# Kernel optimization log

Hardware: AMD Instinct MI355X
Metric: run time of the kernel (lower is better)

Reference implementation:

```python
import jax, jax.numpy as jnp
from jax import lax
import numpy as np

B, CIN, HC, K, REC = 64, 64, 64, 3, 5
MG = 240 // REC  # 48
EPS = 1e-8


def conv2d(x, w, b, pad):
    y = lax.conv_general_dilated(x, w, (1, 1), [(pad, pad), (pad, pad)],
                                 dimension_numbers=('NCHW', 'OIHW', 'NCHW'))
    return y + b[None, :, None, None]


def conv_transpose2d(x, w, b, stride, pad):
    # PyTorch ConvTranspose2d: w is (Cin, Cout, kH, kW)
    k = w.shape[2]
    w_t = jnp.transpose(w[:, :, ::-1, ::-1], (1, 0, 2, 3))  # -> OIHW, flipped
    y = lax.conv_general_dilated(x, w_t, (1, 1),
                                 [(k - 1 - pad, k - 1 - pad)] * 2,
                                 lhs_dilation=(stride, stride),
                                 dimension_numbers=('NCHW', 'OIHW', 'NCHW'))
    return y + b[None, :, None, None]


def leaky(x):
    return jnp.where(x >= 0, x, 0.2 * x)


def setup_inputs() -> dict:
    key = jax.random.key(0)
    ks = jax.random.split(key, 12)
    s = 0.05
    return {
        'x': jax.random.normal(ks[0], (B, CIN, 64, 64), jnp.float32),
        'h': jax.random.normal(ks[1], (B, HC, 64, 64), jnp.float32),
        'c': jax.random.normal(ks[2], (B, HC, 64, 64), jnp.float32),
        'recalled_memory_feature': jax.random.normal(ks[3], (B, REC, MG, 32, 32), jnp.float32),
        'conv_w': jax.random.normal(ks[4], (5 * HC, CIN + HC, K, K), jnp.float32) * s,
        'conv_b': jax.random.normal(ks[5], (5 * HC,), jnp.float32) * s,
        'convc_w': jax.random.normal(ks[6], (MG, HC, 1, 1), jnp.float32) * s,
        'convc_b': jax.random.normal(ks[7], (MG,), jnp.float32) * s,
        'convssm_w': jax.random.normal(ks[8], (MG, MG, 4, 4), jnp.float32) * s,
        'convssm_b': jax.random.normal(ks[9], (MG,), jnp.float32) * s,
        'convfuse_w': jax.random.normal(ks[10], (HC, MG + HC, 1, 1), jnp.float32) * s,
        'convfuse_b': jax.random.normal(ks[11], (HC,), jnp.float32) * s,
    }


def reference(x, h, c, recalled_memory_feature, conv_w, conv_b, convc_w, convc_b,
              convssm_w, convssm_b, convfuse_w, convfuse_b):
    rm = recalled_memory_feature.reshape(B, REC, MG, 32, 32)
    rm_avg = rm.mean(axis=(3, 4))                      # (B, REC, MG)
    q = leaky(conv2d(c, convc_w, convc_b, 0))          # (B, MG, 64, 64)
    q_avg = q.mean(axis=(2, 3))                        # (B, MG)
    # cosine similarity along channel dim, vectorized over (B, REC)
    qn = jnp.maximum(jnp.linalg.norm(q_avg, axis=1, keepdims=True), EPS)   # (B,1)
    mn = jnp.maximum(jnp.linalg.norm(rm_avg, axis=2), EPS)                  # (B,REC)
    cos = jnp.einsum('bm,brm->br', q_avg, rm_avg) / (qn * mn)               # (B,REC)
    attn = jax.nn.softmax(cos, axis=1)                                      # (B,REC)
    mt = jnp.einsum('br,brmhw->bmhw', attn, rm)        # (B, MG, 32, 32)
    mt = leaky(conv_transpose2d(mt, convssm_w, convssm_b, 2, 1))  # (B, MG, 64, 64)

    gates = conv2d(jnp.concatenate((x, h), axis=1), conv_w, conv_b, K // 2)
    i, f, g, o, lam = jnp.split(gates, 5, axis=1)
    i = jax.nn.sigmoid(i)
    f = jax.nn.sigmoid(f)
    o = jax.nn.sigmoid(o)
    g = jnp.tanh(g)
    lam = jax.nn.sigmoid(lam)
    c_new = f * c + i * g
    h_new = o * jnp.tanh(conv2d(jnp.concatenate((c_new, mt), axis=1), convfuse_w, convfuse_b, 0))
    h_out = lam * h_new + (1.0 - lam) * h
    return (h_out, c_new)
```

## Files before the change

### kernel.cpp

```cpp
#include <hip/hip_runtime.h>
#include <hip/hip_bf16.h>
#include <cstdint>

#define HW 4096
#define MGc 48
#define RECc 5

typedef __attribute__((ext_vector_type(8))) short bf16x8;
typedef __attribute__((ext_vector_type(4))) float f32x4;

__device__ __forceinline__ float sigf(float x) { return 1.f / (1.f + expf(-x)); }
__device__ __forceinline__ float leakyf(float x) { return x >= 0.f ? x : 0.2f * x; }
__device__ __forceinline__ unsigned short f2bfu(float f) {
  __hip_bfloat16 b = __float2bfloat16(f);
  return *reinterpret_cast<unsigned short*>(&b);
}
__device__ __forceinline__ float bfu2f(unsigned short u) {
  unsigned v = ((unsigned)u) << 16;
  return __uint_as_float(v);
}
__device__ __forceinline__ void gload_lds16(const void* g, void* l) {
  __builtin_amdgcn_global_load_lds(
      (const __attribute__((address_space(1))) unsigned int*)g,
      (__attribute__((address_space(3))) unsigned int*)l, 16, 0, 0);
}

__global__ __launch_bounds__(256) void k_prep(const float* __restrict__ cw,
    __hip_bfloat16* __restrict__ Wp, __hip_bfloat16* __restrict__ Pp) {
  if (blockIdx.x < 1440) {
    int idx = blockIdx.x * 256 + threadIdx.x;
    int t = idx / (320 * 128);
    int rem = idx % (320 * 128);
    int ocp = rem / 128, ci = rem % 128;
    int nt = ocp / 80, r2 = ocp % 80, gate = r2 / 16, ml = r2 % 16;
    int oc = gate * 64 + nt * 16 + ml;
    Wp[idx] = __float2bfloat16(cw[((size_t)oc * 128 + ci) * 9 + t]);
  } else {
    int idx = (blockIdx.x - 1440) * 256 + threadIdx.x;
    int b = idx / 4160, i = idx % 4160;
    bf16x8* base = reinterpret_cast<bf16x8*>(Pp);
    size_t u;
    if (i < 2112) {
      int r = (i < 1056) ? 0 : 65;
      int j = (i < 1056) ? i : i - 1056;
      u = ((size_t)b * 66 + r) * 1056 + j;
    } else {
      int i2 = i - 2112;
      int row = 1 + (i2 >> 5), k = i2 & 31;
      int px = (k < 16) ? 0 : 65, ci8 = k & 15;
      u = (((size_t)b * 66 + row) * 66 + px) * 16 + ci8;
    }
    base[u] = (bf16x8)0;
  }
}

__global__ __launch_bounds__(256) void k_rm_sum(const float* __restrict__ rm,
                                                float* __restrict__ rm_sum) {
  int row = blockIdx.x;
  const float4* p = reinterpret_cast<const float4*>(rm + (size_t)row * 1024);
  float4 v = p[threadIdx.x];
  float s = v.x + v.y + v.z + v.w;
  #pragma unroll
  for (int off = 32; off; off >>= 1) s += __shfl_down(s, off);
  __shared__ float sred[4];
  if ((threadIdx.x & 63) == 0) sred[threadIdx.x >> 6] = s;
  __syncthreads();
  if (threadIdx.x == 0) rm_sum[row] = sred[0] + sred[1] + sred[2] + sred[3];
}

__global__ __launch_bounds__(256) void k_q_part(const float* __restrict__ c,
    const float* __restrict__ ccw, const float* __restrict__ ccb,
    float* __restrict__ q_part) {
  __shared__ float wl[MGc * 64];
  __shared__ float bl[MGc];
  __shared__ float red[4][MGc];
  int b = blockIdx.y, seg = blockIdx.x;
  for (int i = threadIdx.x; i < MGc * 64; i += 256) wl[i] = ccw[i];
  if (threadIdx.x < MGc) bl[threadIdx.x] = ccb[threadIdx.x];
  __syncthreads();
  int px = seg * 256 + threadIdx.x;
  float acc[MGc];
  #pragma unroll
  for (int m = 0; m < MGc; m++) acc[m] = 0.f;
  const float* cp = c + (size_t)b * 64 * HW + px;
  for (int ci = 0; ci < 64; ci++) {
    float v = cp[(size_t)ci * HW];
    #pragma unroll
    for (int m = 0; m < MGc; m++) acc[m] += wl[m * 64 + ci] * v;
  }
  int lane = threadIdx.x & 63, wv = threadIdx.x >> 6;
  #pragma unroll
  for (int m = 0; m < MGc; m++) {
    float t = leakyf(acc[m] + bl[m]);
    #pragma unroll
    for (int off = 32; off; off >>= 1) t += __shfl_down(t, off);
    if (lane == 0) red[wv][m] = t;
  }
  __syncthreads();
  if (threadIdx.x < MGc) {
    float t = red[0][threadIdx.x] + red[1][threadIdx.x] + red[2][threadIdx.x] + red[3][threadIdx.x];
    q_part[((size_t)b * 16 + seg) * MGc + threadIdx.x] = t;
  }
}

__global__ __launch_bounds__(256) void k_mt_pre(const float* __restrict__ rm,
    const float* __restrict__ rm_sum, const float* __restrict__ q_part,
    float* __restrict__ mt_pre) {
  __shared__ float sat[RECc];
  int idx = blockIdx.x * 256 + threadIdx.x;
  int b = idx / (MGc * 1024);
  if (threadIdx.x < 64) {
    int lane = threadIdx.x;
    float q = 0.f;
    if (lane < MGc) {
      float s = 0.f;
      for (int sg = 0; sg < 16; sg++) s += q_part[((size_t)b * 16 + sg) * MGc + lane];
      q = s * (1.f / 4096.f);
    }
    float qs = q * q;
    #pragma unroll
    for (int off = 32; off; off >>= 1) qs += __shfl_xor(qs, off);
    float qn = fmaxf(sqrtf(qs), 1e-8f);
    float cosv[RECc];
    #pragma unroll
    for (int r = 0; r < RECc; r++) {
      float m = 0.f;
      if (lane < MGc) m = rm_sum[((size_t)b * RECc + r) * MGc + lane] * (1.f / 1024.f);
      float d = q * m, ms = m * m;
      #pragma unroll
      for (int off = 32; off; off >>= 1) { d += __shfl_xor(d, off); ms += __shfl_xor(ms, off); }
      float mn = fmaxf(sqrtf(ms), 1e-8f);
      cosv[r] = d / (qn * mn);
    }
    float mx = cosv[0];
    #pragma unroll
    for (int r = 1; r < RECc; r++) mx = fmaxf(mx, cosv[r]);
    float ssum = 0.f;
    #pragma unroll
    for (int r = 0; r < RECc; r++) { cosv[r] = expf(cosv[r] - mx); ssum += cosv[r]; }
    float inv = 1.f / ssum;
    #pragma unroll
    for (int r = 0; r < RECc; r++)
      if (lane == r) sat[r] = cosv[r] * inv;
  }
  __syncthreads();
  int rem = idx - b * (MGc * 1024);
  const float* base = rm + (size_t)b * RECc * MGc * 1024 + rem;
  float v = sat[0] * base[0] + sat[1] * base[MGc * 1024] + sat[2] * base[2 * MGc * 1024]
          + sat[3] * base[3 * MGc * 1024] + sat[4] * base[4 * MGc * 1024];
  mt_pre[idx] = v;
}

__global__ __launch_bounds__(512) void k_ssm(const float* __restrict__ mt_pre,
    const float* __restrict__ w, const float* __restrict__ bias,
    __hip_bfloat16* __restrict__ mt) {
  __shared__ float in_t[12][10][20];
  __shared__ float w_t[12][48][16];
  int b = blockIdx.y;
  int tile = blockIdx.x;
  int y0 = (tile >> 1) * 16, x0 = (tile & 1) * 32;
  int wv = threadIdx.x >> 6, lane = threadIdx.x & 63;
  int co0 = wv * 6;
  int oyl = lane >> 2, xseg = lane & 3;
  int oy = y0 + oyl;
  int iy0 = (y0 >> 1) - 1, ix0 = (x0 >> 1) - 1;
  int kyA = (oy + 1) & 1;
  int iyA = (oy + 1 - kyA) >> 1;
  int rA = iyA - iy0, rB = rA - 1;
  float acc[6][8] = {};
  for (int ch = 0; ch < 4; ch++) {
    int ci0 = ch * 12;
    __syncthreads();
    for (int i = threadIdx.x; i < 12 * 10 * 18; i += 512) {
      int ci = i / 180, rr = (i % 180) / 18, cc2 = i % 18;
      int giy = iy0 + rr, gix = ix0 + cc2;
      float v = 0.f;
      if ((unsigned)giy < 32u && (unsigned)gix < 32u)
        v = mt_pre[(((size_t)b * MGc + ci0 + ci) * 32 + giy) * 32 + gix];
      in_t[ci][rr][cc2] = v;
    }
    for (int i = threadIdx.x; i < 12 * 48 * 16; i += 512)
      (&w_t[0][0][0])[i] = w[ci0 * 768 + i];
    __syncthreads();
    #pragma unroll 1
    for (int ci = 0; ci < 12; ci++) {
      float4 a0 = *reinterpret_cast<const float4*>(&in_t[ci][rA][xseg * 4]);
      float4 a1 = *reinterpret_cast<const float4*>(&in_t[ci][rA][xseg * 4 + 4]);
      float4 b0 = *reinterpret_cast<const float4*>(&in_t[ci][rB][xseg * 4]);
      float4 b1 = *reinterpret_cast<const float4*>(&in_t[ci][rB][xseg * 4 + 4]);
      float vA[6] = {a0.x, a0.y, a0.z, a0.w, a1.x, a1.y};
      float vB[6] = {b0.x, b0.y, b0.z, b0.w, b1.x, b1.y};
      #pragma unroll
      for (int co = 0; co < 6; co++) {
        const float* wp = &w_t[ci][co0 + co][0];
        float4 wA = *reinterpret_cast<const float4*>(wp + kyA * 4);
        float4 wB = *reinterpret_cast<const float4*>(wp + (kyA + 2) * 4);
        #pragma unroll
        for (int j = 0; j < 8; j++) {
          if ((j & 1) == 0) {
            int hi = (j >> 1) + 1, lo = j >> 1;
            acc[co][j] += vA[hi] * wA.y + vA[lo] * wA.w + vB[hi] * wB.y + vB[lo] * wB.w;
          } else {
            int hi = ((j + 1) >> 1) + 1, lo = (j + 1) >> 1;
            acc[co][j] += vA[hi] * wA.x + vA[lo] * wA.z + vB[hi] * wB.x + vB[lo] * wB.z;
          }
        }
      }
    }
  }
  int oxb = x0 + xseg * 8;
  #pragma unroll
  for (int co = 0; co < 6; co++) {
    float bb = bias[co0 + co];
    size_t obase = (((size_t)b * MGc + co0 + co) * 64 + oy) * 64 + oxb;
    #pragma unroll
    for (int j = 0; j < 8; j++)
      mt[obase + j] = __float2bfloat16(leakyf(acc[co][j] + bb));
  }
}

__global__ __launch_bounds__(256) void k_ppack(const float* __restrict__ xin,
    const float* __restrict__ hin, __hip_bfloat16* __restrict__ Pp) {
  __shared__ float t[64][65];
  int b = blockIdx.z, y = blockIdx.y, half = blockIdx.x;
  const float* src = (half ? hin : xin) + (size_t)b * 64 * HW + y * 64;
  #pragma unroll
  for (int it = 0; it < 4; it++) {
    int li = it * 256 + threadIdx.x;
    int ci = li >> 4, x4 = (li & 15) * 4;
    float4 v = *reinterpret_cast<const float4*>(src + (size_t)ci * HW + x4);
    t[x4][ci] = v.x; t[x4 + 1][ci] = v.y; t[x4 + 2][ci] = v.z; t[x4 + 3][ci] = v.w;
  }
  __syncthreads();
  int x = threadIdx.x >> 2, c16 = (threadIdx.x & 3) * 16;
  unsigned short* dst = reinterpret_cast<unsigned short*>(Pp) +
      ((((size_t)b * 66 + y + 1) * 66 + x + 1) * 128 + half * 64 + c16);
  bf16x8 o0, o1;
  #pragma unroll
  for (int j = 0; j < 8; j++) {
    o0[j] = (short)f2bfu(t[x][c16 + j]);
    o1[j] = (short)f2bfu(t[x][c16 + 8 + j]);
  }
  *reinterpret_cast<bf16x8*>(dst) = o0;
  *reinterpret_cast<bf16x8*>(dst + 8) = o1;
}

__global__ __launch_bounds__(512) void k_gates_mfma(
    const __hip_bfloat16* __restrict__ Pp, const __hip_bfloat16* __restrict__ Wp,
    const float* __restrict__ c, const float* __restrict__ cb,
    float* __restrict__ c_new, __hip_bfloat16* __restrict__ o_g,
    __hip_bfloat16* __restrict__ lam_g) {
  __shared__ bf16x8 s_w[9 * 4 * 80];
  int orig = blockIdx.y * gridDim.x + blockIdx.x;
  int t_id = (orig & 7) * 128 + (orig >> 3);
  int b = t_id >> 4;
  int ytile = (t_id >> 2) & 3, nt = t_id & 3;
  int y0 = ytile * 16;
  int tid = threadIdx.x;
  int wv = tid >> 6, lane = tid & 63;
  int wr = wv >> 2, xw = wv & 3;
  int lane15 = lane & 15, lq = lane >> 4;

  const char* Ab = (const char*)Pp +
      ((((size_t)b * 66 + (y0 + wr * 8)) * 66 + (xw * 16 + lane15)) * 256) + lq * 16;

  f32x4 acc[8][5];
  #pragma unroll
  for (int i = 0; i < 8; i++)
    #pragma unroll
    for (int j = 0; j < 5; j++) acc[i][j] = (f32x4)0.f;

  const char* Wb = (const char*)Wp;

#define COMP(AF, DX) do {                                                             \
    _Pragma("unroll")                                                                 \
    for (int ky = 0; ky < 3; ky++) {                                                  \
      int t = ky * 3 + (DX);                                                          \
      bf16x8 bw[5];                                                                   \
      _Pragma("unroll")                                                               \
      for (int gg = 0; gg < 5; gg++) bw[gg] = s_w[(t * 4 + lq) * 80 + gg * 16 + lane15]; \
      __builtin_amdgcn_s_setprio(1);                                                  \
      _Pragma("unroll")                                                               \
      for (int rr = 0; rr < 8; rr++)                                                  \
        _Pragma("unroll")                                                             \
        for (int gg = 0; gg < 5; gg++)                                                \
          acc[rr][gg] = __builtin_amdgcn_mfma_f32_16x16x32_bf16(                      \
              AF[rr + ky], bw[gg], acc[rr][gg], 0, 0, 0);                             \
      __builtin_amdgcn_s_setprio(0);                                                  \
    }                                                                                 \
  } while (0)

  #pragma unroll 1
  for (int cc = 0; cc < 4; cc++) {
    __syncthreads();
    #pragma unroll 1
    for (int u = wv; u < 45; u += 8) {
      int e = u * 64 + lane;
      int t = e / 320, rem = e % 320;
      int g = rem / 80, ol = rem % 80;
      const char* gp = Wb + (((size_t)t * 320 + nt * 80 + ol) * 128 + cc * 32 + g * 8) * 2;
      gload_lds16(gp, (void*)&s_w[e]);
    }
    const char* Ac = Ab + cc * 64;
    bf16x8 afA[10], afB[10];
    #pragma unroll
    for (int ri = 0; ri < 10; ri++)
      afA[ri] = *reinterpret_cast<const bf16x8*>(Ac + ri * 16896);
    __syncthreads();
    #pragma unroll
    for (int ri = 0; ri < 10; ri++)
      afB[ri] = *reinterpret_cast<const bf16x8*>(Ac + ri * 16896 + 256);
    COMP(afA, 0);
    #pragma unroll
    for (int ri = 0; ri < 10; ri++)
      afA[ri] = *reinterpret_cast<const bf16x8*>(Ac + ri * 16896 + 512);
    COMP(afB, 1);
    COMP(afA, 2);
  }
#undef COMP

  int m_hid = nt * 16 + lane15;
  float bi = cb[m_hid], bff = cb[64 + m_hid], bgg = cb[128 + m_hid],
        bo = cb[192 + m_hid], bl = cb[256 + m_hid];
  int xb = xw * 16 + lq * 4;
  size_t chofs = ((size_t)b * 64 + m_hid) * HW;
  #pragma unroll
  for (int rr = 0; rr < 8; rr++) {
    int y = y0 + wr * 8 + rr;
    size_t pofs = chofs + (size_t)y * 64 + xb;
    f32x4 cold = *reinterpret_cast<const f32x4*>(c + pofs);
    f32x4 cn;
    unsigned short ov[4], lv[4];
    #pragma unroll
    for (int e = 0; e < 4; e++) {
      float i_ = sigf(acc[rr][0][e] + bi);
      float f_ = sigf(acc[rr][1][e] + bff);
      float g_ = tanhf(acc[rr][2][e] + bgg);
      float o_ = sigf(acc[rr][3][e] + bo);
      float l_ = sigf(acc[rr][4][e] + bl);
      cn[e] = f_ * cold[e] + i_ * g_;
      ov[e] = f2bfu(o_);
      lv[e] = f2bfu(l_);
    }
    *reinterpret_cast<f32x4*>(c_new + pofs) = cn;
    ushort4 ovv = {ov[0], ov[1], ov[2], ov[3]};
    ushort4 lvv = {lv[0], lv[1], lv[2], lv[3]};
    *reinterpret_cast<ushort4*>(reinterpret_cast<unsigned short*>(o_g) + pofs) = ovv;
    *reinterpret_cast<ushort4*>(reinterpret_cast<unsigned short*>(lam_g) + pofs) = lvv;
  }
}

__global__ __launch_bounds__(256) void k_fuse(const float* __restrict__ c_new,
    const __hip_bfloat16* __restrict__ mt, const __hip_bfloat16* __restrict__ o_g,
    const __hip_bfloat16* __restrict__ lam_g, const float* __restrict__ h,
    const float* __restrict__ fw, const float* __restrict__ fb,
    float* __restrict__ h_out) {
  __shared__ float wl[112][64];
  int b = blockIdx.y, seg = blockIdx.x;
  for (int i = threadIdx.x; i < 112 * 64; i += 256) {
    int ci = i >> 6, co = i & 63;
    wl[ci][co] = fw[co * 112 + ci];
  }
  __syncthreads();
  int px = seg * 512 + threadIdx.x * 2;
  size_t bofs = (size_t)b * 64 * HW;
  float2 acc[64];
  #pragma unroll
  for (int co = 0; co < 64; co++) { float bv = fb[co]; acc[co].x = bv; acc[co].y = bv; }
  #pragma unroll 1
  for (int ci = 0; ci < 64; ci++) {
    float2 v = *reinterpret_cast<const float2*>(c_new + bofs + (size_t)ci * HW + px);
    #pragma unroll
    for (int c4 = 0; c4 < 16; c4++) {
      float4 w = *reinterpret_cast<const float4*>(&wl[ci][c4 * 4]);
      acc[c4 * 4 + 0].x += w.x * v.x; acc[c4 * 4 + 0].y += w.x * v.y;
      acc[c4 * 4 + 1].x += w.y * v.x; acc[c4 * 4 + 1].y += w.y * v.y;
      acc[c4 * 4 + 2].x += w.z * v.x; acc[c4 * 4 + 2].y += w.z * v.y;
      acc[c4 * 4 + 3].x += w.w * v.x; acc[c4 * 4 + 3].y += w.w * v.y;
    }
  }
  const unsigned short* mtu = reinterpret_cast<const unsigned short*>(mt);
  size_t mtofs = (size_t)b * MGc * HW + px;
  #pragma unroll 1
  for (int ci = 0; ci < 48; ci++) {
    unsigned u = *reinterpret_cast<const unsigned*>(mtu + mtofs + (size_t)ci * HW);
    float vx = bfu2f((unsigned short)(u & 0xffff));
    float vy = bfu2f((unsigned short)(u >> 16));
    #pragma unroll
    for (int c4 = 0; c4 < 16; c4++) {
      float4 w = *reinterpret_cast<const float4*>(&wl[64 + ci][c4 * 4]);
      acc[c4 * 4 + 0].x += w.x * vx; acc[c4 * 4 + 0].y += w.x * vy;
      acc[c4 * 4 + 1].x += w.y * vx; acc[c4 * 4 + 1].y += w.y * vy;
      acc[c4 * 4 + 2].x += w.z * vx; acc[c4 * 4 + 2].y += w.z * vy;
      acc[c4 * 4 + 3].x += w.w * vx; acc[c4 * 4 + 3].y += w.w * vy;
    }
  }
  const unsigned short* ou = reinterpret_cast<const unsigned short*>(o_g);
  const unsigned short* lu = reinterpret_cast<const unsigned short*>(lam_g);
  #pragma unroll
  for (int co = 0; co < 64; co++) {
    size_t ofs = bofs + (size_t)co * HW + px;
    unsigned uo = *reinterpret_cast<const unsigned*>(ou + ofs);
    unsigned ul = *reinterpret_cast<const unsigned*>(lu + ofs);
    float2 hv = *reinterpret_cast<const float2*>(h + ofs);
    float hnx = tanhf(acc[co].x), hny = tanhf(acc[co].y);
    float ox = bfu2f((unsigned short)(uo & 0xffff)), oy = bfu2f((unsigned short)(uo >> 16));
    float lx = bfu2f((unsigned short)(ul & 0xffff)), ly = bfu2f((unsigned short)(ul >> 16));
    float2 r;
    r.x = lx * (ox * hnx) + (1.f - lx) * hv.x;
    r.y = ly * (oy * hny) + (1.f - ly) * hv.y;
    *reinterpret_cast<float2*>(h_out + ofs) = r;
  }
}

extern "C" void kernel_launch(void* const* d_in, const int* in_sizes, int n_in,
                              void* d_out, int out_size, void* d_ws, size_t ws_size,
                              hipStream_t stream) {
  const float* x   = (const float*)d_in[0];
  const float* h   = (const float*)d_in[1];
  const float* c   = (const float*)d_in[2];
  const float* rm  = (const float*)d_in[3];
  const float* cw  = (const float*)d_in[4];
  const float* cb  = (const float*)d_in[5];
  const float* ccw = (const float*)d_in[6];
  const float* ccb = (const float*)d_in[7];
  const float* sw  = (const float*)d_in[8];
  const float* sb  = (const float*)d_in[9];
  const float* fw  = (const float*)d_in[10];
  const float* fb  = (const float*)d_in[11];

  float* h_out = (float*)d_out;
  float* c_new = h_out + (size_t)16777216;

  char* ws = (char*)d_ws;
  float* rm_sum = (float*)(ws + 0);
  float* q_part = (float*)(ws + 65536);
  float* mt_pre = (float*)(ws + 262144);
  __hip_bfloat16* o_g   = (__hip_bfloat16*)(ws + 0);
  __hip_bfloat16* lam_g = (__hip_bfloat16*)(ws + 33554432);
  __hip_bfloat16* mt    = (__hip_bfloat16*)(ws + 67108864);
  __hip_bfloat16* Pp    = (__hip_bfloat16*)(ws + 92274688);
  __hip_bfloat16* Wp    = (__hip_bfloat16*)(ws + 163643392);

  k_prep<<<2480, 256, 0, stream>>>(cw, Wp, Pp);
  k_ppack<<<dim3(2, 64, 64), 256, 0, stream>>>(x, h, Pp);
  k_rm_sum<<<15360, 256, 0, stream>>>(rm, rm_sum);
  k_q_part<<<dim3(16, 64), 256, 0, stream>>>(c, ccw, ccb, q_part);
  k_mt_pre<<<12288, 256, 0, stream>>>(rm, rm_sum, q_part, mt_pre);
  k_ssm<<<dim3(8, 64), 512, 0, stream>>>(mt_pre, sw, sb, mt);
  k_gates_mfma<<<dim3(16, 64), 512, 0, stream>>>(Pp, Wp, c, cb, c_new, o_g, lam_g);
  k_fuse<<<dim3(8, 64), 256, 0, stream>>>(c_new, mt, o_g, lam_g, h, fw, fb, h_out);
}
```

Measured before the change: 783.7 us.

## Stage gates conv input halo tile in LDS with smaller 16x16 spatial tiles

The gates convolution kernel now works on 16x16 spatial tiles with 4 waves instead of 16-row tiles with 8 waves. The padded input halo is staged into shared memory via global_load_lds instead of each wave loading A fragments directly from global memory per row. The launch grid grows fourfold with fewer accumulators per wave, which cuts register pressure and raises occupancy. In exchange each tile reloads the full weight slice for every 16x16 tile, so weight traffic into LDS goes up, and the halo overlap between tiles adds redundant input reads.

```diff
diff --git a/kernel.cpp b/kernel.cpp
--- a/kernel.cpp
+++ b/kernel.cpp
@@ -245,88 +245,89 @@
   *reinterpret_cast<bf16x8*>(dst + 8) = o1;
 }
 
-__global__ __launch_bounds__(512) void k_gates_mfma(
+__global__ __launch_bounds__(256) void k_gates_mfma(
     const __hip_bfloat16* __restrict__ Pp, const __hip_bfloat16* __restrict__ Wp,
     const float* __restrict__ c, const float* __restrict__ cb,
     float* __restrict__ c_new, __hip_bfloat16* __restrict__ o_g,
     __hip_bfloat16* __restrict__ lam_g) {
+  __shared__ bf16x8 s_in[18 * 4 * 18];
   __shared__ bf16x8 s_w[9 * 4 * 80];
   int orig = blockIdx.y * gridDim.x + blockIdx.x;
-  int t_id = (orig & 7) * 128 + (orig >> 3);
-  int b = t_id >> 4;
-  int ytile = (t_id >> 2) & 3, nt = t_id & 3;
-  int y0 = ytile * 16;
+  int t_id = (orig & 7) * 512 + (orig >> 3);
+  int b = t_id >> 6;
+  int r6 = t_id & 63;
+  int ytile = r6 >> 4, xtile = (r6 >> 2) & 3, nt = r6 & 3;
+  int y0 = ytile * 16, x0 = xtile * 16;
   int tid = threadIdx.x;
   int wv = tid >> 6, lane = tid & 63;
-  int wr = wv >> 2, xw = wv & 3;
   int lane15 = lane & 15, lq = lane >> 4;
 
-  const char* Ab = (const char*)Pp +
-      ((((size_t)b * 66 + (y0 + wr * 8)) * 66 + (xw * 16 + lane15)) * 256) + lq * 16;
-
-  f32x4 acc[8][5];
-  #pragma unroll
-  for (int i = 0; i < 8; i++)
+  f32x4 acc[4][5];
+  #pragma unroll
+  for (int i = 0; i < 4; i++)
     #pragma unroll
     for (int j = 0; j < 5; j++) acc[i][j] = (f32x4)0.f;
 
+  const char* Pb = (const char*)Pp;
   const char* Wb = (const char*)Wp;
-
-#define COMP(AF, DX) do {                                                             \
-    _Pragma("unroll")                                                                 \
-    for (int ky = 0; ky < 3; ky++) {                                                  \
-      int t = ky * 3 + (DX);                                                          \
-      bf16x8 bw[5];                                                                   \
-      _Pragma("unroll")                                                               \
-      for (int gg = 0; gg < 5; gg++) bw[gg] = s_w[(t * 4 + lq) * 80 + gg * 16 + lane15]; \
-      __builtin_amdgcn_s_setprio(1);                                                  \
-      _Pragma("unroll")                                                               \
-      for (int rr = 0; rr < 8; rr++)                                                  \
-        _Pragma("unroll")                                                             \
-        for (int gg = 0; gg < 5; gg++)                                                \
-          acc[rr][gg] = __builtin_amdgcn_mfma_f32_16x16x32_bf16(                      \
-              AF[rr + ky], bw[gg], acc[rr][gg], 0, 0, 0);                             \
-      __builtin_amdgcn_s_setprio(0);                                                  \
-    }                                                                                 \
-  } while (0)
 
   #pragma unroll 1
   for (int cc = 0; cc < 4; cc++) {
     __syncthreads();
     #pragma unroll 1
-    for (int u = wv; u < 45; u += 8) {
+    for (int u = wv; u < 21; u += 4) {
       int e = u * 64 + lane;
-      int t = e / 320, rem = e % 320;
-      int g = rem / 80, ol = rem % 80;
+      if (e < 1296) {
+        int L = e / 72, r = e - L * 72;
+        int llq = r / 18, xi = r - llq * 18;
+        const char* gp = Pb + ((((size_t)b * 66 + y0 + L) * 66 + (x0 + xi)) * 256)
+                         + cc * 64 + llq * 16;
+        gload_lds16(gp, (void*)&s_in[e]);
+      }
+    }
+    #pragma unroll 1
+    for (int u = wv; u < 45; u += 4) {
+      int e = u * 64 + lane;
+      int unit = e / 80, ol = e - unit * 80;
+      int t = unit >> 2, g = unit & 3;
       const char* gp = Wb + (((size_t)t * 320 + nt * 80 + ol) * 128 + cc * 32 + g * 8) * 2;
       gload_lds16(gp, (void*)&s_w[e]);
     }
-    const char* Ac = Ab + cc * 64;
-    bf16x8 afA[10], afB[10];
-    #pragma unroll
-    for (int ri = 0; ri < 10; ri++)
-      afA[ri] = *reinterpret_cast<const bf16x8*>(Ac + ri * 16896);
     __syncthreads();
-    #pragma unroll
-    for (int ri = 0; ri < 10; ri++)
-      afB[ri] = *reinterpret_cast<const bf16x8*>(Ac + ri * 16896 + 256);
-    COMP(afA, 0);
-    #pragma unroll
-    for (int ri = 0; ri < 10; ri++)
-      afA[ri] = *reinterpret_cast<const bf16x8*>(Ac + ri * 16896 + 512);
-    COMP(afB, 1);
-    COMP(afA, 2);
-  }
-#undef COMP
+
+    #pragma unroll
+    for (int dx = 0; dx < 3; dx++) {
+      #pragma unroll
+      for (int ky = 0; ky < 3; ky++) {
+        int t = ky * 3 + dx;
+        bf16x8 af[4];
+        #pragma unroll
+        for (int rr = 0; rr < 4; rr++)
+          af[rr] = s_in[((wv * 4 + rr + ky) * 4 + lq) * 18 + lane15 + dx];
+        bf16x8 bw[5];
+        #pragma unroll
+        for (int gg = 0; gg < 5; gg++)
+          bw[gg] = s_w[(t * 4 + lq) * 80 + gg * 16 + lane15];
+        __builtin_amdgcn_s_setprio(1);
+        #pragma unroll
+        for (int rr = 0; rr < 4; rr++)
+          #pragma unroll
+          for (int gg = 0; gg < 5; gg++)
+            acc[rr][gg] = __builtin_amdgcn_mfma_f32_16x16x32_bf16(
+                af[rr], bw[gg], acc[rr][gg], 0, 0, 0);
+        __builtin_amdgcn_s_setprio(0);
+      }
+    }
+  }
 
   int m_hid = nt * 16 + lane15;
   float bi = cb[m_hid], bff = cb[64 + m_hid], bgg = cb[128 + m_hid],
         bo = cb[192 + m_hid], bl = cb[256 + m_hid];
-  int xb = xw * 16 + lq * 4;
+  int xb = x0 + lq * 4;
   size_t chofs = ((size_t)b * 64 + m_hid) * HW;
   #pragma unroll
-  for (int rr = 0; rr < 8; rr++) {
-    int y = y0 + wr * 8 + rr;
+  for (int rr = 0; rr < 4; rr++) {
+    int y = y0 + wv * 4 + rr;
     size_t pofs = chofs + (size_t)y * 64 + xb;
     f32x4 cold = *reinterpret_cast<const f32x4*>(c + pofs);
     f32x4 cn;
@@ -448,6 +449,6 @@
   k_q_part<<<dim3(16, 64), 256, 0, stream>>>(c, ccw, ccb, q_part);
   k_mt_pre<<<12288, 256, 0, stream>>>(rm, rm_sum, q_part, mt_pre);
   k_ssm<<<dim3(8, 64), 512, 0, stream>>>(mt_pre, sw, sb, mt);
-  k_gates_mfma<<<dim3(16, 64), 512, 0, stream>>>(Pp, Wp, c, cb, c_new, o_g, lam_g);
+  k_gates_mfma<<<dim3(64, 64), 256, 0, stream>>>(Pp, Wp, c, cb, c_new, o_g, lam_g);
   k_fuse<<<dim3(8, 64), 256, 0, stream>>>(c_new, mt, o_g, lam_g, h, fw, fb, h_out);
 }
```

New measurement: 637.1 us. 18.7% less time.
